# Kernel optimization log

Hardware: AMD Instinct MI355X
Metric: run time of the kernel (lower is better)

The kernel has to match this reference:

```python
import jax, jax.numpy as jnp
import numpy as np

B, T, OMNI_D, STATIC_D = 128, 1024, 32, 16
H = 64            # hidden // 2 (per-direction GRU size)
HID = 128         # hidden
PHYS_LEN, N_PHYS = 432, 5


def _gelu(x):
    return jax.nn.gelu(x, approximate=False)  # torch GELU default = exact erf


def _ln(x, g, b, eps=1e-5):
    m = jnp.mean(x, -1, keepdims=True)
    v = jnp.var(x, -1, keepdims=True)
    return (x - m) / jnp.sqrt(v + eps) * g + b


def _gru_layer(x, Wih, Whh, bih, bhh, reverse):
    # PyTorch GRU cell math; x: [B,T,D] -> (outputs [B,T,H], h_final [B,H])
    Hh = Whh.shape[1]
    gi = jnp.einsum('btd,gd->btg', x, Wih) + bih  # precompute input projections
    if reverse:
        gi = gi[:, ::-1]
    gi = jnp.swapaxes(gi, 0, 1)  # [T,B,3H]
    h0 = jnp.zeros((x.shape[0], Hh), x.dtype)

    def step(h, g):
        gh = h @ Whh.T + bhh
        r = jax.nn.sigmoid(g[:, :Hh] + gh[:, :Hh])
        z = jax.nn.sigmoid(g[:, Hh:2 * Hh] + gh[:, Hh:2 * Hh])
        n = jnp.tanh(g[:, 2 * Hh:] + r * gh[:, 2 * Hh:])
        hn = (1 - z) * n + z * h
        return hn, hn

    hT, ys = jax.lax.scan(step, h0, gi)
    ys = jnp.swapaxes(ys, 0, 1)
    if reverse:
        ys = ys[:, ::-1]
    return ys, hT


def _conv1d(x, W, b, pad, dil):
    y = jax.lax.conv_general_dilated(x, W, (1,), [(pad, pad)], rhs_dilation=(dil,),
                                     dimension_numbers=('NCH', 'OIH', 'NCH'))
    return y + b[None, :, None]


def setup_inputs():
    key = jax.random.key(0)
    ks = iter(jax.random.split(key, 64))

    def rn(shape, s=0.05):
        return jax.random.normal(next(ks), shape, jnp.float32) * s

    inp = {
        'omni_seq': rn((B, T, OMNI_D), 1.0),
        'static_x': rn((B, STATIC_D), 1.0),
        'phys': rn((B, N_PHYS, PHYS_LEN), 1.0),
    }
    for l, d_in in (('l0', OMNI_D), ('l1', 2 * H)):
        for dr in ('f', 'b'):
            inp[f'gru_Wih_{l}{dr}'] = rn((3 * H, d_in))
            inp[f'gru_Whh_{l}{dr}'] = rn((3 * H, H))
            inp[f'gru_bih_{l}{dr}'] = rn((3 * H,))
            inp[f'gru_bhh_{l}{dr}'] = rn((3 * H,))
    inp['sm_W'] = rn((H, STATIC_D)); inp['sm_b'] = rn((H,))
    inp['sm_ln_g'] = jnp.ones((H,), jnp.float32); inp['sm_ln_b'] = jnp.zeros((H,), jnp.float32)
    inp['gate_W'] = rn((N_PHYS, H)); inp['gate_b'] = rn((N_PHYS,))
    inp['attn_in_W'] = rn((3 * N_PHYS, N_PHYS)); inp['attn_in_b'] = rn((3 * N_PHYS,))
    inp['attn_out_W'] = rn((N_PHYS, N_PHYS)); inp['attn_out_b'] = rn((N_PHYS,))
    for i, ksz in ((1, 3), (2, 5), (3, 9)):
        inp[f'conv{i}_W'] = rn((HID // 4, N_PHYS, ksz)); inp[f'conv{i}_b'] = rn((HID // 4,))
    FUSED = HID + H + 3 * (HID // 4)  # 288
    inp['head_ln_g'] = jnp.ones((FUSED,), jnp.float32); inp['head_ln_b'] = jnp.zeros((FUSED,), jnp.float32)
    inp['head_W1'] = rn((HID, FUSED)); inp['head_b1'] = rn((HID,))
    inp['head_W2'] = rn((PHYS_LEN, HID)); inp['head_b2'] = rn((PHYS_LEN,))
    return inp


def reference(omni_seq, static_x, phys,
              gru_Wih_l0f, gru_Whh_l0f, gru_bih_l0f, gru_bhh_l0f,
              gru_Wih_l0b, gru_Whh_l0b, gru_bih_l0b, gru_bhh_l0b,
              gru_Wih_l1f, gru_Whh_l1f, gru_bih_l1f, gru_bhh_l1f,
              gru_Wih_l1b, gru_Whh_l1b, gru_bih_l1b, gru_bhh_l1b,
              sm_W, sm_b, sm_ln_g, sm_ln_b, gate_W, gate_b,
              attn_in_W, attn_in_b, attn_out_W, attn_out_b,
              conv1_W, conv1_b, conv2_W, conv2_b, conv3_W, conv3_b,
              head_ln_g, head_ln_b, head_W1, head_b1, head_W2, head_b2):
    # --- bidirectional 2-layer GRU (eval mode: dropout off) ---
    y0f, _ = _gru_layer(omni_seq, gru_Wih_l0f, gru_Whh_l0f, gru_bih_l0f, gru_bhh_l0f, False)
    y0b, _ = _gru_layer(omni_seq, gru_Wih_l0b, gru_Whh_l0b, gru_bih_l0b, gru_bhh_l0b, True)
    x1 = jnp.concatenate([y0f, y0b], -1)
    _, hf = _gru_layer(x1, gru_Wih_l1f, gru_Whh_l1f, gru_bih_l1f, gru_bhh_l1f, False)
    _, hb = _gru_layer(x1, gru_Wih_l1b, gru_Whh_l1b, gru_bih_l1b, gru_bhh_l1b, True)
    omni_embed = jnp.concatenate([hf, hb], -1)  # h_omni[-2] ++ h_omni[-1], [B,128]
    # --- static MLP ---
    static_embed = _ln(_gelu(static_x @ sm_W.T + sm_b), sm_ln_g, sm_ln_b)  # [B,64]
    # --- gating on phys channels ---
    gates = jax.nn.sigmoid(static_embed @ gate_W.T + gate_b)[..., None]  # [B,5,1]
    p = phys * gates  # [B,5,432]
    # --- tiny MHA: embed_dim=5, 5 heads, head_dim=1 -> scale = 1/sqrt(1) = 1 ---
    pt = jnp.swapaxes(p, 1, 2)  # [B,432,5]
    qkv = pt @ attn_in_W.T + attn_in_b
    E = N_PHYS
    q, k, v = qkv[..., :E], qkv[..., E:2 * E], qkv[..., 2 * E:]
    scores = jnp.einsum('bih,bjh->bhij', q, k)  # [B,5,432,432]
    attn = jax.nn.softmax(scores, -1)
    ao = jnp.einsum('bhij,bjh->bih', attn, v)
    ao = ao @ attn_out_W.T + attn_out_b  # out_proj
    p = jnp.swapaxes(ao, 1, 2)  # [B,5,432]
    # --- dilated conv branches + GELU + adaptive avg pool (= mean over length) ---
    c1 = _gelu(_conv1d(p, conv1_W, conv1_b, 1, 1)).mean(-1)
    c2 = _gelu(_conv1d(p, conv2_W, conv2_b, 2, 2)).mean(-1)
    c3 = _gelu(_conv1d(p, conv3_W, conv3_b, 4, 4)).mean(-1)
    fused = jnp.concatenate([omni_embed, static_embed, c1, c2, c3], 1)  # [B,288]
    h = _ln(fused, head_ln_g, head_ln_b)
    h = _gelu(h @ head_W1.T + head_b1)  # dropout off in eval
    return h @ head_W2.T + head_b2  # [B,432]
```

## Files before the change

### kernel.cpp

```cpp
#include <hip/hip_runtime.h>
#include <stdint.h>

#define B_ 128
#define T_ 1024
#define BT_ (B_*T_)
#define H_ 64
#define G_ 192
#define PL_ 432
#define NP_ 5
#define FUSED_ 288
#define N_IN 41
#define NSTATIC 128
#define NRECUR 256
#define NGEMM 2048

typedef unsigned short u16;
typedef __attribute__((ext_vector_type(8))) short bf16x8;
typedef __attribute__((ext_vector_type(4))) float f32x4;
typedef _Float16 h2 __attribute__((ext_vector_type(2)));
typedef _Float16 h8 __attribute__((ext_vector_type(8)));

__device__ inline float bf2f(u16 u){ union{float f; unsigned int i;} c; c.i = ((unsigned int)u)<<16; return c.f; }
__device__ inline u16 f2bf(float f){ unsigned int u = __float_as_uint(f); unsigned int r = (u + 0x7fffu + ((u>>16)&1u))>>16; return (u16)r; }
__device__ inline _Float16 bf2h(u16 u){ return (_Float16)bf2f(u); }
__device__ inline float sigm(float x){ return 1.f/(1.f+__expf(-x)); }
__device__ inline float tanh_(float x){ float t = __expf(fminf(fmaxf(2.f*x,-30.f),30.f)); return (t-1.f)/(t+1.f); }
__device__ inline float gelu_(float x){ return 0.5f*x*(1.f + erff(x*0.70710678118654752f)); }
__device__ inline float wredsum(float v){
  #pragma unroll
  for(int o=32;o>0;o>>=1) v += __shfl_xor(v,o);
  return v;
}

#if __has_builtin(__builtin_amdgcn_fdot2)
__device__ inline float dot2(h2 a, h2 b, float c){ return __builtin_amdgcn_fdot2(a, b, c, false); }
#else
__device__ inline float dot2(h2 a, h2 b, float c){ return c + (float)a.x*(float)b.x + (float)a.y*(float)b.y; }
#endif

struct CvtArgs {
  const void* src[N_IN];
  unsigned dstOff[N_IN];
  unsigned cnt[N_IN];
  unsigned blkStart[N_IN+1];
};

__global__ __launch_bounds__(256) void convert_k(CvtArgs a, u16* __restrict__ dst,
                                                 unsigned* __restrict__ flags){
  int b = blockIdx.x;
  if ((unsigned)b >= a.blkStart[N_IN]){
    unsigned base = ((unsigned)b - a.blkStart[N_IN])*2048u;
    #pragma unroll
    for(int e=0;e<8;e++){ unsigned idx = base + e*256u + threadIdx.x; if (idx < 4096u) flags[idx] = 0u; }
    return;
  }
  const bool isbf = (((const u16*)a.src[21])[0] == 0x3F80u);
  int lo = 0, hi = N_IN;
  while (hi - lo > 1){ int mid = (lo+hi)>>1; if (a.blkStart[mid] <= (unsigned)b) lo = mid; else hi = mid; }
  const int i = lo;
  const unsigned lb = (unsigned)b - a.blkStart[i];
  const unsigned n = a.cnt[i];
  u16* d = dst + a.dstOff[i];
  if (isbf){
    const u16* s = (const u16*)a.src[i];
    #pragma unroll
    for(int e=0;e<8;e++){ unsigned idx = lb*2048u + e*256u + threadIdx.x; if (idx < n) d[idx] = s[idx]; }
  } else {
    const float* s = (const float*)a.src[i];
    #pragma unroll
    for(int e=0;e<8;e++){ unsigned idx = lb*2048u + e*256u + threadIdx.x; if (idx < n) d[idx] = f2bf(s[idx]); }
  }
}

template<int LAYER>
__device__ void recur_body(int chain, const u16* gi,
    const u16* __restrict__ WhF, const u16* __restrict__ WhB,
    const u16* __restrict__ bhF, const u16* __restrict__ bhB,
    u16* __restrict__ y_x1, float* __restrict__ hfin,
    const unsigned* flags)
{
  const int dir = chain >> 7;
  const int b = chain & 127;
  const int j = threadIdx.x;
  const u16* Wh = dir ? WhB : WhF;
  const u16* bh = dir ? bhB : bhF;

  h2 wr[32], wz[32], wn[32];
  #pragma unroll
  for(int k8=0;k8<8;k8++){
    uint4 q;
    q = *(const uint4*)(Wh + (size_t)j*64 + k8*8);
    wr[4*k8+0] = (h2){bf2h((u16)(q.x&0xffffu)), bf2h((u16)(q.x>>16))};
    wr[4*k8+1] = (h2){bf2h((u16)(q.y&0xffffu)), bf2h((u16)(q.y>>16))};
    wr[4*k8+2] = (h2){bf2h((u16)(q.z&0xffffu)), bf2h((u16)(q.z>>16))};
    wr[4*k8+3] = (h2){bf2h((u16)(q.w&0xffffu)), bf2h((u16)(q.w>>16))};
    q = *(const uint4*)(Wh + (size_t)(64+j)*64 + k8*8);
    wz[4*k8+0] = (h2){bf2h((u16)(q.x&0xffffu)), bf2h((u16)(q.x>>16))};
    wz[4*k8+1] = (h2){bf2h((u16)(q.y&0xffffu)), bf2h((u16)(q.y>>16))};
    wz[4*k8+2] = (h2){bf2h((u16)(q.z&0xffffu)), bf2h((u16)(q.z>>16))};
    wz[4*k8+3] = (h2){bf2h((u16)(q.w&0xffffu)), bf2h((u16)(q.w>>16))};
    q = *(const uint4*)(Wh + (size_t)(128+j)*64 + k8*8);
    wn[4*k8+0] = (h2){bf2h((u16)(q.x&0xffffu)), bf2h((u16)(q.x>>16))};
    wn[4*k8+1] = (h2){bf2h((u16)(q.y&0xffffu)), bf2h((u16)(q.y>>16))};
    wn[4*k8+2] = (h2){bf2h((u16)(q.z&0xffffu)), bf2h((u16)(q.z>>16))};
    wn[4*k8+3] = (h2){bf2h((u16)(q.w&0xffffu)), bf2h((u16)(q.w>>16))};
  }
  const float bhr = bf2f(bh[j]), bhz = bf2f(bh[64+j]), bhn = bf2f(bh[128+j]);

  __shared__ __align__(16) u16 giLds[2][3072];
  __shared__ _Float16 hSf[64];
  h8* hS8 = (h8*)hSf;
  hSf[j] = (_Float16)0.f;

  const u16* giC = gi + (size_t)chain * T_ * G_;

  auto issue_chunk = [&](int c, int buf){
    int tbase = dir ? (1008 - c*16) : (c*16);
    const u16* src = giC + (size_t)tbase*G_ + j*8;
    u16* dst = &giLds[buf][0];
    #pragma unroll
    for(int i=0;i<6;i++){
      __builtin_amdgcn_global_load_lds(
        (const __attribute__((address_space(1))) void*)(src + i*512),
        (__attribute__((address_space(3))) void*)(dst + i*512), 16, 0, 0);
    }
  };

  int readyTile = -1;
  auto wait_tile = [&](int c){
    int tbase = dir ? (1008 - c*16) : (c*16);
    int tile = tbase >> 6;
    if (tile == readyTile) return;
    const unsigned* f = &flags[b*16 + tile];
    while (__hip_atomic_load(f, __ATOMIC_ACQUIRE, __HIP_MEMORY_SCOPE_AGENT) == 0u)
      __builtin_amdgcn_s_sleep(2);
    readyTile = tile;
  };

  wait_tile(0);
  issue_chunk(0, 0);

  float h = 0.f;
  for(int c=0; c<64; ++c){
    if (c < 63) wait_tile(c+1);
    asm volatile("s_waitcnt vmcnt(0)" ::: "memory");
    if (c < 63) issue_chunk(c+1, (c+1)&1);
    const u16* gbuf = &giLds[c&1][0];
    #pragma unroll 2
    for(int ls=0; ls<16; ++ls){
      int row = dir ? (15-ls) : ls;
      const u16* rowp = gbuf + row*G_;
      float r0=bhr, r1=0.f, z0=bhz, z1=0.f, n0=bhn, n1=0.f;
      #pragma unroll
      for(int k=0;k<8;k++){
        h8 hv = hS8[k];
        h2 p0 = __builtin_shufflevector(hv, hv, 0, 1);
        h2 p1 = __builtin_shufflevector(hv, hv, 2, 3);
        h2 p2 = __builtin_shufflevector(hv, hv, 4, 5);
        h2 p3 = __builtin_shufflevector(hv, hv, 6, 7);
        r0 = dot2(wr[4*k+0], p0, r0); r1 = dot2(wr[4*k+1], p1, r1);
        r0 = dot2(wr[4*k+2], p2, r0); r1 = dot2(wr[4*k+3], p3, r1);
        z0 = dot2(wz[4*k+0], p0, z0); z1 = dot2(wz[4*k+1], p1, z1);
        z0 = dot2(wz[4*k+2], p2, z0); z1 = dot2(wz[4*k+3], p3, z1);
        n0 = dot2(wn[4*k+0], p0, n0); n1 = dot2(wn[4*k+1], p1, n1);
        n0 = dot2(wn[4*k+2], p2, n0); n1 = dot2(wn[4*k+3], p3, n1);
      }
      float gr = bf2f(rowp[j]), gz = bf2f(rowp[64+j]), gn = bf2f(rowp[128+j]);

      float r  = sigm(gr + (r0+r1));
      float z  = sigm(gz + (z0+z1));
      float nn = tanh_(gn + r*(n0+n1));
      h = (1.f - z)*nn + z*h;

      hSf[j] = (_Float16)h;

      if (LAYER == 0){
        int s = c*16 + ls;
        int t = dir ? (T_-1-s) : s;
        y_x1[((size_t)b*T_ + t)*128 + dir*64 + j] = f2bf(h);
      }
    }
  }
  if (LAYER == 1) hfin[b*FUSED_ + dir*64 + j] = h;
}

__device__ inline int tile_order(int tslot){ return (tslot & 1) ? (15 - (tslot >> 1)) : (tslot >> 1); }

__device__ inline void publish_flag(unsigned* flags, int idx){
  __syncthreads();
  if (threadIdx.x == 0){
    __threadfence();
    __hip_atomic_store(&flags[idx], 1u, __ATOMIC_RELEASE, __HIP_MEMORY_SCOPE_AGENT);
  }
}

__global__ __launch_bounds__(256,1) void fused0_k(
    const void* __restrict__ Araw,
    const u16* __restrict__ Wf, const u16* __restrict__ Wb,
    const u16* __restrict__ biasF, const u16* __restrict__ biasB,
    u16* gi,
    const u16* __restrict__ WhF, const u16* __restrict__ WhB,
    const u16* __restrict__ bhF, const u16* __restrict__ bhB,
    u16* __restrict__ y_x1, unsigned* flags, const u16* __restrict__ detect)
{
  if (blockIdx.x < NRECUR){
    if (threadIdx.x < 64)
      recur_body<0>(blockIdx.x, gi, WhF, WhB, bhF, bhB, y_x1, nullptr, flags);
    return;
  }
  const bool isbf = (detect[0] == 0x3F80u);
  const int g = blockIdx.x - NRECUR;
  const int bb = g & 127;
  const int ttile = tile_order(g >> 7);
  const int wv = threadIdx.x >> 6, lane = threadIdx.x & 63;
  const int l15 = lane & 15, quad = lane >> 4;
  const size_t mBase = ((size_t)bb*16 + ttile)*64 + wv*16;

  bf16x8 afr;
  if (isbf){
    afr = *(const bf16x8*)((const u16*)Araw + (mBase + l15)*32 + quad*8);
  } else {
    const float* af = (const float*)Araw + (mBase + l15)*32 + quad*8;
    float4 f0 = *(const float4*)af;
    float4 f1 = *(const float4*)(af+4);
    union { bf16x8 v; u16 e[8]; } u_;
    u_.e[0]=f2bf(f0.x); u_.e[1]=f2bf(f0.y); u_.e[2]=f2bf(f0.z); u_.e[3]=f2bf(f0.w);
    u_.e[4]=f2bf(f1.x); u_.e[5]=f2bf(f1.y); u_.e[6]=f2bf(f1.z); u_.e[7]=f2bf(f1.w);
    afr = u_.v;
  }

  #pragma unroll
  for(int half=0; half<2; ++half){
    const u16* W    = half ? Wb : Wf;
    const u16* bias = half ? biasB : biasF;
    u16* o = gi + (size_t)half * BT_ * G_;
    for(int nt=0; nt<12; ++nt){
      int n = nt*16 + l15;
      f32x4 acc = {0.f,0.f,0.f,0.f};
      bf16x8 bfr = *(const bf16x8*)(W + n*32 + quad*8);
      acc = __builtin_amdgcn_mfma_f32_16x16x32_bf16(bfr, afr, acc, 0,0,0);
      ushort4 bb4 = *(const ushort4*)(bias + nt*16 + quad*4);
      ushort4 pk;
      pk.x = f2bf(acc[0] + bf2f(bb4.x));
      pk.y = f2bf(acc[1] + bf2f(bb4.y));
      pk.z = f2bf(acc[2] + bf2f(bb4.z));
      pk.w = f2bf(acc[3] + bf2f(bb4.w));
      *(ushort4*)(o + (mBase + l15)*G_ + nt*16 + quad*4) = pk;
    }
  }
  publish_flag(flags, bb*16 + ttile);
}

template<int KS, int DIL, int PAD>
__device__ inline void do_conv(const float* pS, const u16* Wc, const u16* bc,
                               float* fused, int b, int o, int p, int cslot)
{
  const int Lout = PL_ + 2*PAD - DIL*(KS-1);
  float w[5][KS];
  #pragma unroll
  for(int i=0;i<5;i++)
    #pragma unroll
    for(int t=0;t<KS;t++) w[i][t] = bf2f(Wc[(o*5+i)*KS + t]);
  float bias = bf2f(bc[o]);
  float acc = 0.f;
  for(int l=p; l<Lout; l+=8){
    float s = bias;
    #pragma unroll
    for(int t=0;t<KS;t++){
      int idx = l - PAD + t*DIL;
      if (idx >= 0 && idx < PL_){
        #pragma unroll
        for(int i=0;i<5;i++) s += w[i][t]*pS[i*PL_ + idx];
      }
    }
    acc += gelu_(s);
  }
  #pragma unroll
  for(int off=1;off<8;off<<=1) acc += __shfl_xor(acc,off);
  if (p == 0) fused[b*FUSED_ + 192 + cslot*32 + o] = acc/(float)Lout;
}

__device__ void static_body(int b, int tid,
   const u16* sx, const u16* smW, const u16* smb,
   const u16* lng, const u16* lnb, const u16* gW, const u16* gb,
   const void* physRaw, const u16* aW, const u16* ab,
   const u16* oW, const u16* ob,
   const u16* W1c, const u16* b1c, const u16* W2c, const u16* b2c,
   const u16* W3c, const u16* b3c,
   float* fused, bool isbf)
{
  __shared__ float qS[15*PL_];
  __shared__ float aoS[PL_*5];
  __shared__ float gS[5];
  __shared__ float redS[40];
  __shared__ float kmS[5], knS[5];

  if (tid < 64){
    int j = tid;
    float acc = bf2f(smb[j]);
    #pragma unroll
    for(int k=0;k<16;k++) acc += bf2f(sx[b*16+k])*bf2f(smW[j*16+k]);
    float xg = gelu_(acc);
    float m = wredsum(xg)*(1.f/64.f);
    float d = xg - m;
    float v = wredsum(d*d)*(1.f/64.f);
    float se = d*rsqrtf(v+1e-5f)*bf2f(lng[j]) + bf2f(lnb[j]);
    fused[b*FUSED_ + 128 + j] = se;
    #pragma unroll
    for(int i=0;i<5;i++){
      float p = se*bf2f(gW[i*64+j]);
      float s = wredsum(p);
      if (j == 0) gS[i] = sigm(s + bf2f(gb[i]));
    }
  }
  __syncthreads();

  for(int l=tid; l<PL_; l+=256){
    float pv[5];
    #pragma unroll
    for(int i=0;i<5;i++){
      size_t idx = ((size_t)b*5+i)*PL_ + l;
      float pr = isbf ? bf2f(((const u16*)physRaw)[idx]) : ((const float*)physRaw)[idx];
      pv[i] = pr * gS[i];
    }
    #pragma unroll
    for(int c=0;c<15;c++){
      float a = bf2f(ab[c]);
      #pragma unroll
      for(int i=0;i<5;i++) a += pv[i]*bf2f(aW[c*5+i]);
      qS[c*PL_ + l] = a;
    }
  }
  __syncthreads();

  float mx[5], mn[5];
  #pragma unroll
  for(int h=0;h<5;h++){ mx[h]=-1e30f; mn[h]=1e30f; }
  for(int jj=tid; jj<PL_; jj+=256){
    #pragma unroll
    for(int h=0;h<5;h++){ float kv=qS[(5+h)*PL_+jj]; mx[h]=fmaxf(mx[h],kv); mn[h]=fminf(mn[h],kv); }
  }
  #pragma unroll
  for(int o=32;o>0;o>>=1){
    #pragma unroll
    for(int h=0;h<5;h++){ mx[h]=fmaxf(mx[h],__shfl_xor(mx[h],o)); mn[h]=fminf(mn[h],__shfl_xor(mn[h],o)); }
  }
  int wv = tid>>6;
  if ((tid&63)==0){
    #pragma unroll
    for(int h=0;h<5;h++){ redS[wv*10+h]=mx[h]; redS[wv*10+5+h]=mn[h]; }
  }
  __syncthreads();
  if (tid < 5){
    float a=redS[tid], c=redS[5+tid];
    for(int w2=1;w2<4;w2++){ a=fmaxf(a,redS[w2*10+tid]); c=fminf(c,redS[w2*10+5+tid]); }
    kmS[tid]=a; knS[tid]=c;
  }
  __syncthreads();

  for(int i=tid; i<PL_; i+=256){
    #pragma unroll
    for(int h=0;h<5;h++){
      float s = qS[h*PL_+i];
      float m = fmaxf(s*kmS[h], s*knS[h]);
      const float* kR = &qS[(5+h)*PL_];
      const float* vR = &qS[(10+h)*PL_];
      float den=0.f, num=0.f;
      #pragma unroll 4
      for(int j2=0;j2<PL_;j2++){
        float e = __expf(s*kR[j2]-m);
        den += e; num += e*vR[j2];
      }
      aoS[i*5+h] = num/den;
    }
  }
  __syncthreads();

  float* pS = qS;
  for(int l=tid; l<PL_; l+=256){
    float a[5];
    #pragma unroll
    for(int hh=0;hh<5;hh++) a[hh] = aoS[l*5+hh];
    #pragma unroll
    for(int c=0;c<5;c++){
      float s = bf2f(ob[c]);
      #pragma unroll
      for(int hh=0;hh<5;hh++) s += a[hh]*bf2f(oW[c*5+hh]);
      pS[c*PL_ + l] = s;
    }
  }
  __syncthreads();

  int o = tid >> 3, p = tid & 7;
  do_conv<3,1,1>(pS, W1c, b1c, fused, b, o, p, 0);
  do_conv<5,2,2>(pS, W2c, b2c, fused, b, o, p, 1);
  do_conv<9,4,4>(pS, W3c, b3c, fused, b, o, p, 2);
}

__global__ __launch_bounds__(256,1) void fused1_k(
    const u16* __restrict__ A,
    const u16* __restrict__ Wf, const u16* __restrict__ Wb,
    const u16* __restrict__ biasF, const u16* __restrict__ biasB,
    u16* gi,
    const u16* __restrict__ WhF, const u16* __restrict__ WhB,
    const u16* __restrict__ bhF, const u16* __restrict__ bhB,
    float* __restrict__ fusedOut, unsigned* flags,
    const u16* __restrict__ sx, const u16* __restrict__ smW, const u16* __restrict__ smb,
    const u16* __restrict__ lng, const u16* __restrict__ lnb,
    const u16* __restrict__ gW, const u16* __restrict__ gb,
    const void* __restrict__ physRaw, const u16* __restrict__ aW, const u16* __restrict__ ab,
    const u16* __restrict__ oW, const u16* __restrict__ ob,
    const u16* __restrict__ W1c, const u16* __restrict__ b1c,
    const u16* __restrict__ W2c, const u16* __restrict__ b2c,
    const u16* __restrict__ W3c, const u16* __restrict__ b3c,
    const u16* __restrict__ detect)
{
  const bool isbf = (detect[0] == 0x3F80u);
  if (blockIdx.x < NRECUR){
    if (threadIdx.x < 64)
      recur_body<1>(blockIdx.x, gi, WhF, WhB, bhF, bhB, nullptr, fusedOut, flags);
    return;
  }
  if (blockIdx.x >= NRECUR + NGEMM){
    static_body(blockIdx.x - (NRECUR + NGEMM), threadIdx.x,
                sx, smW, smb, lng, lnb, gW, gb, physRaw, aW, ab,
                oW, ob, W1c, b1c, W2c, b2c, W3c, b3c, fusedOut, isbf);
    return;
  }
  const int g = blockIdx.x - NRECUR;
  const int bb = g & 127;
  const int ttile = tile_order(g >> 7);
  const int wv = threadIdx.x >> 6, lane = threadIdx.x & 63;
  const int l15 = lane & 15, quad = lane >> 4;
  const size_t mBase = ((size_t)bb*16 + ttile)*64 + wv*16;

  bf16x8 afr[4];
  #pragma unroll
  for(int kc=0;kc<4;kc++)
    afr[kc] = *(const bf16x8*)(A + (mBase + l15)*128 + kc*32 + quad*8);

  #pragma unroll
  for(int half=0; half<2; ++half){
    const u16* W    = half ? Wb : Wf;
    const u16* bias = half ? biasB : biasF;
    u16* o = gi + (size_t)half * BT_ * G_;
    for(int nt=0; nt<12; ++nt){
      int n = nt*16 + l15;
      f32x4 acc = {0.f,0.f,0.f,0.f};
      #pragma unroll
      for(int kc=0;kc<4;kc++){
        bf16x8 bfr = *(const bf16x8*)(W + n*128 + kc*32 + quad*8);
        acc = __builtin_amdgcn_mfma_f32_16x16x32_bf16(bfr, afr[kc], acc, 0,0,0);
      }
      ushort4 bb4 = *(const ushort4*)(bias + nt*16 + quad*4);
      ushort4 pk;
      pk.x = f2bf(acc[0] + bf2f(bb4.x));
      pk.y = f2bf(acc[1] + bf2f(bb4.y));
      pk.z = f2bf(acc[2] + bf2f(bb4.z));
      pk.w = f2bf(acc[3] + bf2f(bb4.w));
      *(ushort4*)(o + (mBase + l15)*G_ + nt*16 + quad*4) = pk;
    }
  }
  publish_flag(flags, bb*16 + ttile);
}

__global__ __launch_bounds__(448) void head_k(const float* __restrict__ fused,
   const u16* __restrict__ lng, const u16* __restrict__ lnb,
   const u16* __restrict__ W1, const u16* __restrict__ b1,
   const u16* __restrict__ W2, const u16* __restrict__ b2,
   void* __restrict__ out, const u16* __restrict__ detect)
{
  const bool isbf = (detect[0] == 0x3F80u);
  int b = blockIdx.x, tid = threadIdx.x;
  __shared__ float fS[FUSED_];
  __shared__ float hS[128];
  __shared__ float red[32];
  float v = (tid < FUSED_) ? fused[b*FUSED_ + tid] : 0.f;
  float s1 = wredsum(v);
  float s2 = wredsum(v*v);
  int wv = tid>>6;
  if ((tid&63)==0){ red[wv]=s1; red[8+wv]=s2; }
  __syncthreads();
  if (tid==0){
    float S=0.f, SS=0.f;
    for(int i=0;i<7;i++){ S+=red[i]; SS+=red[8+i]; }
    float m = S/288.f;
    red[16]=m; red[17]=SS/288.f - m*m;
  }
  __syncthreads();
  float m = red[16], var = red[17];
  if (tid < FUSED_) fS[tid] = (v-m)*rsqrtf(var+1e-5f)*bf2f(lng[tid]) + bf2f(lnb[tid]);
  __syncthreads();
  if (tid < 128){
    float a = bf2f(b1[tid]);
    const u16* wr = W1 + (size_t)tid*FUSED_;
    #pragma unroll
    for(int k8=0;k8<36;k8++){
      uint4 q = *(const uint4*)(wr + k8*8);
      a += fS[8*k8+0]*bf2f((u16)(q.x&0xffffu)) + fS[8*k8+1]*bf2f((u16)(q.x>>16))
         + fS[8*k8+2]*bf2f((u16)(q.y&0xffffu)) + fS[8*k8+3]*bf2f((u16)(q.y>>16))
         + fS[8*k8+4]*bf2f((u16)(q.z&0xffffu)) + fS[8*k8+5]*bf2f((u16)(q.z>>16))
         + fS[8*k8+6]*bf2f((u16)(q.w&0xffffu)) + fS[8*k8+7]*bf2f((u16)(q.w>>16));
    }
    hS[tid] = gelu_(a);
  }
  __syncthreads();
  if (tid < PL_){
    float a = bf2f(b2[tid]);
    const u16* wr = W2 + (size_t)tid*128;
    #pragma unroll
    for(int k8=0;k8<16;k8++){
      uint4 q = *(const uint4*)(wr + k8*8);
      a += hS[8*k8+0]*bf2f((u16)(q.x&0xffffu)) + hS[8*k8+1]*bf2f((u16)(q.x>>16))
         + hS[8*k8+2]*bf2f((u16)(q.y&0xffffu)) + hS[8*k8+3]*bf2f((u16)(q.y>>16))
         + hS[8*k8+4]*bf2f((u16)(q.z&0xffffu)) + hS[8*k8+5]*bf2f((u16)(q.z>>16))
         + hS[8*k8+6]*bf2f((u16)(q.w&0xffffu)) + hS[8*k8+7]*bf2f((u16)(q.w>>16));
    }
    size_t oi = (size_t)b*PL_ + tid;
    if (isbf) ((u16*)out)[oi] = f2bf(a);
    else      ((float*)out)[oi] = a;
  }
}

extern "C" void kernel_launch(void* const* d_in, const int* in_sizes, int n_in,
                              void* d_out, int out_size, void* d_ws, size_t ws_size,
                              hipStream_t stream)
{
  static const unsigned cnts[N_IN] = {
    4194304, 2048, 276480,
    6144, 12288, 192, 192,
    6144, 12288, 192, 192,
    24576, 12288, 192, 192,
    24576, 12288, 192, 192,
    1024, 64, 64, 64,
    320, 5,
    75, 15,
    25, 5,
    480, 32, 800, 32, 1440, 32,
    288, 288,
    36864, 128, 55296, 432
  };

  char* ws = (char*)d_ws;
  size_t off = 0;
  auto alloc = [&](size_t bytes){ size_t o = off; off = (off + bytes + 255) & ~(size_t)255; return o; };

  CvtArgs ca;
  const u16* cin[N_IN];
  unsigned totalBlocks = 0;
  for (int i=0;i<N_IN;i++){
    ca.src[i] = d_in[i];
    ca.cnt[i] = cnts[i];
    size_t o = alloc((size_t)cnts[i]*2);
    ca.dstOff[i] = (unsigned)(o/2);
    cin[i] = (const u16*)(ws + o);
    ca.blkStart[i] = totalBlocks;
    if (i != 0 && i != 2) totalBlocks += (cnts[i] + 2047u)/2048u;
  }
  ca.blkStart[N_IN] = totalBlocks;
  u16* canon = (u16*)ws;

  u16*   gi    = (u16*)  (ws + alloc((size_t)2*BT_*G_*2));
  u16*   x1    = (u16*)  (ws + alloc((size_t)BT_*128*2));
  float* fused = (float*)(ws + alloc((size_t)B_*FUSED_*4));
  unsigned* flags = (unsigned*)(ws + alloc((size_t)4096*4));
  (void)ws_size; (void)in_sizes; (void)n_in; (void)out_size;

  convert_k<<<totalBlocks + 2, 256, 0, stream>>>(ca, canon, flags);

  fused0_k<<<NRECUR + NGEMM, 256, 0, stream>>>(d_in[0],
      cin[3], cin[7], cin[5], cin[9], gi,
      cin[4], cin[8], cin[6], cin[10], x1, flags, (const u16*)d_in[21]);

  fused1_k<<<NRECUR + NGEMM + NSTATIC, 256, 0, stream>>>(x1,
      cin[11], cin[15], cin[13], cin[17], gi,
      cin[12], cin[16], cin[14], cin[18], fused, flags + 2048,
      cin[1], cin[19], cin[20], cin[21], cin[22], cin[23], cin[24],
      d_in[2], cin[25], cin[26],
      cin[27], cin[28], cin[29], cin[30], cin[31], cin[32], cin[33], cin[34],
      (const u16*)d_in[21]);

  head_k<<<128, 448, 0, stream>>>(fused, cin[35], cin[36], cin[37], cin[38], cin[39], cin[40],
                                  d_out, (const u16*)d_in[21]);
}
```

Baseline: 1.414 ms.

## Shrink fused GRU/GEMM/static blocks to single-wavefront workgroups

Both fused kernels now launch 64-thread blocks instead of 256. GEMM blocks loop over the four 16-row M sub-tiles inside one wave, and the static branch (attention, out-projection, dilated convs) is rewritten for one wave with fewer LDS buffers and barriers. The aim is to stop recurrence blocks from occupying three idle waves and to let more blocks be resident, which should help the flag-based producer/consumer pipelining. The cost is less parallelism per GEMM and static block, which lengthens the static branch, and the block barrier before the flag publish is removed.

Measured after the change: 1.667 ms. 1.18x slower.

```diff
diff --git a/kernel.cpp b/kernel.cpp
--- a/kernel.cpp
+++ b/kernel.cpp
@@ -187,14 +187,14 @@
 __device__ inline int tile_order(int tslot){ return (tslot & 1) ? (15 - (tslot >> 1)) : (tslot >> 1); }
 
 __device__ inline void publish_flag(unsigned* flags, int idx){
-  __syncthreads();
-  if (threadIdx.x == 0){
-    __threadfence();
+  __threadfence();
+  if (threadIdx.x == 0)
     __hip_atomic_store(&flags[idx], 1u, __ATOMIC_RELEASE, __HIP_MEMORY_SCOPE_AGENT);
-  }
-}
-
-__global__ __launch_bounds__(256,1) void fused0_k(
+}
+
+__global__ __launch_bounds__(64)
+__attribute__((amdgpu_waves_per_eu(1,1)))
+void fused0_k(
     const void* __restrict__ Araw,
     const u16* __restrict__ Wf, const u16* __restrict__ Wb,
     const u16* __restrict__ biasF, const u16* __restrict__ biasB,
@@ -204,56 +204,57 @@
     u16* __restrict__ y_x1, unsigned* flags, const u16* __restrict__ detect)
 {
   if (blockIdx.x < NRECUR){
-    if (threadIdx.x < 64)
-      recur_body<0>(blockIdx.x, gi, WhF, WhB, bhF, bhB, y_x1, nullptr, flags);
+    recur_body<0>(blockIdx.x, gi, WhF, WhB, bhF, bhB, y_x1, nullptr, flags);
     return;
   }
   const bool isbf = (detect[0] == 0x3F80u);
   const int g = blockIdx.x - NRECUR;
   const int bb = g & 127;
   const int ttile = tile_order(g >> 7);
-  const int wv = threadIdx.x >> 6, lane = threadIdx.x & 63;
+  const int lane = threadIdx.x;
   const int l15 = lane & 15, quad = lane >> 4;
-  const size_t mBase = ((size_t)bb*16 + ttile)*64 + wv*16;
-
-  bf16x8 afr;
-  if (isbf){
-    afr = *(const bf16x8*)((const u16*)Araw + (mBase + l15)*32 + quad*8);
-  } else {
-    const float* af = (const float*)Araw + (mBase + l15)*32 + quad*8;
-    float4 f0 = *(const float4*)af;
-    float4 f1 = *(const float4*)(af+4);
-    union { bf16x8 v; u16 e[8]; } u_;
-    u_.e[0]=f2bf(f0.x); u_.e[1]=f2bf(f0.y); u_.e[2]=f2bf(f0.z); u_.e[3]=f2bf(f0.w);
-    u_.e[4]=f2bf(f1.x); u_.e[5]=f2bf(f1.y); u_.e[6]=f2bf(f1.z); u_.e[7]=f2bf(f1.w);
-    afr = u_.v;
-  }
 
   #pragma unroll
-  for(int half=0; half<2; ++half){
-    const u16* W    = half ? Wb : Wf;
-    const u16* bias = half ? biasB : biasF;
-    u16* o = gi + (size_t)half * BT_ * G_;
-    for(int nt=0; nt<12; ++nt){
-      int n = nt*16 + l15;
-      f32x4 acc = {0.f,0.f,0.f,0.f};
-      bf16x8 bfr = *(const bf16x8*)(W + n*32 + quad*8);
-      acc = __builtin_amdgcn_mfma_f32_16x16x32_bf16(bfr, afr, acc, 0,0,0);
-      ushort4 bb4 = *(const ushort4*)(bias + nt*16 + quad*4);
-      ushort4 pk;
-      pk.x = f2bf(acc[0] + bf2f(bb4.x));
-      pk.y = f2bf(acc[1] + bf2f(bb4.y));
-      pk.z = f2bf(acc[2] + bf2f(bb4.z));
-      pk.w = f2bf(acc[3] + bf2f(bb4.w));
-      *(ushort4*)(o + (mBase + l15)*G_ + nt*16 + quad*4) = pk;
+  for(int m0=0;m0<4;m0++){
+    const size_t mBase = ((size_t)bb*16 + ttile)*64 + m0*16;
+    bf16x8 afr;
+    if (isbf){
+      afr = *(const bf16x8*)((const u16*)Araw + (mBase + l15)*32 + quad*8);
+    } else {
+      const float* af = (const float*)Araw + (mBase + l15)*32 + quad*8;
+      float4 f0 = *(const float4*)af;
+      float4 f1 = *(const float4*)(af+4);
+      union { bf16x8 v; u16 e[8]; } u_;
+      u_.e[0]=f2bf(f0.x); u_.e[1]=f2bf(f0.y); u_.e[2]=f2bf(f0.z); u_.e[3]=f2bf(f0.w);
+      u_.e[4]=f2bf(f1.x); u_.e[5]=f2bf(f1.y); u_.e[6]=f2bf(f1.z); u_.e[7]=f2bf(f1.w);
+      afr = u_.v;
+    }
+    #pragma unroll
+    for(int half=0; half<2; ++half){
+      const u16* W    = half ? Wb : Wf;
+      const u16* bias = half ? biasB : biasF;
+      u16* o = gi + (size_t)half * BT_ * G_;
+      for(int nt=0; nt<12; ++nt){
+        int n = nt*16 + l15;
+        f32x4 acc = {0.f,0.f,0.f,0.f};
+        bf16x8 bfr = *(const bf16x8*)(W + n*32 + quad*8);
+        acc = __builtin_amdgcn_mfma_f32_16x16x32_bf16(bfr, afr, acc, 0,0,0);
+        ushort4 bb4 = *(const ushort4*)(bias + nt*16 + quad*4);
+        ushort4 pk;
+        pk.x = f2bf(acc[0] + bf2f(bb4.x));
+        pk.y = f2bf(acc[1] + bf2f(bb4.y));
+        pk.z = f2bf(acc[2] + bf2f(bb4.z));
+        pk.w = f2bf(acc[3] + bf2f(bb4.w));
+        *(ushort4*)(o + (mBase + l15)*G_ + nt*16 + quad*4) = pk;
+      }
     }
   }
   publish_flag(flags, bb*16 + ttile);
 }
 
 template<int KS, int DIL, int PAD>
-__device__ inline void do_conv(const float* pS, const u16* Wc, const u16* bc,
-                               float* fused, int b, int o, int p, int cslot)
+__device__ inline void do_conv64(const float* pS, const u16* Wc, const u16* bc,
+                                 float* fused, int b, int o, int p, int cslot)
 {
   const int Lout = PL_ + 2*PAD - DIL*(KS-1);
   float w[5][KS];
@@ -263,7 +264,7 @@
     for(int t=0;t<KS;t++) w[i][t] = bf2f(Wc[(o*5+i)*KS + t]);
   float bias = bf2f(bc[o]);
   float acc = 0.f;
-  for(int l=p; l<Lout; l+=8){
+  for(int l=p; l<Lout; l+=2){
     float s = bias;
     #pragma unroll
     for(int t=0;t<KS;t++){
@@ -275,8 +276,7 @@
     }
     acc += gelu_(s);
   }
-  #pragma unroll
-  for(int off=1;off<8;off<<=1) acc += __shfl_xor(acc,off);
+  acc += __shfl_xor(acc, 32);
   if (p == 0) fused[b*FUSED_ + 192 + cslot*32 + o] = acc/(float)Lout;
 }
 
@@ -290,12 +290,10 @@
    float* fused, bool isbf)
 {
   __shared__ float qS[15*PL_];
-  __shared__ float aoS[PL_*5];
   __shared__ float gS[5];
-  __shared__ float redS[40];
   __shared__ float kmS[5], knS[5];
 
-  if (tid < 64){
+  {
     int j = tid;
     float acc = bf2f(smb[j]);
     #pragma unroll
@@ -315,7 +313,7 @@
   }
   __syncthreads();
 
-  for(int l=tid; l<PL_; l+=256){
+  for(int l=tid; l<PL_; l+=64){
     float pv[5];
     #pragma unroll
     for(int i=0;i<5;i++){
@@ -333,35 +331,30 @@
   }
   __syncthreads();
 
-  float mx[5], mn[5];
-  #pragma unroll
-  for(int h=0;h<5;h++){ mx[h]=-1e30f; mn[h]=1e30f; }
-  for(int jj=tid; jj<PL_; jj+=256){
-    #pragma unroll
-    for(int h=0;h<5;h++){ float kv=qS[(5+h)*PL_+jj]; mx[h]=fmaxf(mx[h],kv); mn[h]=fminf(mn[h],kv); }
-  }
-  #pragma unroll
-  for(int o=32;o>0;o>>=1){
-    #pragma unroll
-    for(int h=0;h<5;h++){ mx[h]=fmaxf(mx[h],__shfl_xor(mx[h],o)); mn[h]=fminf(mn[h],__shfl_xor(mn[h],o)); }
-  }
-  int wv = tid>>6;
-  if ((tid&63)==0){
-    #pragma unroll
-    for(int h=0;h<5;h++){ redS[wv*10+h]=mx[h]; redS[wv*10+5+h]=mn[h]; }
-  }
-  __syncthreads();
-  if (tid < 5){
-    float a=redS[tid], c=redS[5+tid];
-    for(int w2=1;w2<4;w2++){ a=fmaxf(a,redS[w2*10+tid]); c=fminf(c,redS[w2*10+5+tid]); }
-    kmS[tid]=a; knS[tid]=c;
-  }
-  __syncthreads();
-
-  for(int i=tid; i<PL_; i+=256){
+  {
+    float mx[5], mn[5];
+    #pragma unroll
+    for(int h=0;h<5;h++){ mx[h]=-1e30f; mn[h]=1e30f; }
+    for(int jj=tid; jj<PL_; jj+=64){
+      #pragma unroll
+      for(int h=0;h<5;h++){ float kv=qS[(5+h)*PL_+jj]; mx[h]=fmaxf(mx[h],kv); mn[h]=fminf(mn[h],kv); }
+    }
+    #pragma unroll
+    for(int o=32;o>0;o>>=1){
+      #pragma unroll
+      for(int h=0;h<5;h++){ mx[h]=fmaxf(mx[h],__shfl_xor(mx[h],o)); mn[h]=fminf(mn[h],__shfl_xor(mn[h],o)); }
+    }
+    if (tid < 5){ kmS[tid]=mx[tid]; knS[tid]=mn[tid]; }
+  }
+  __syncthreads();
+
+  for(int l=tid; l<PL_; l+=64){
+    float qv[5], aov[5];
+    #pragma unroll
+    for(int h=0;h<5;h++) qv[h] = qS[h*PL_+l];
     #pragma unroll
     for(int h=0;h<5;h++){
-      float s = qS[h*PL_+i];
+      float s = qv[h];
       float m = fmaxf(s*kmS[h], s*knS[h]);
       const float* kR = &qS[(5+h)*PL_];
       const float* vR = &qS[(10+h)*PL_];
@@ -371,33 +364,27 @@
         float e = __expf(s*kR[j2]-m);
         den += e; num += e*vR[j2];
       }
-      aoS[i*5+h] = num/den;
-    }
-  }
-  __syncthreads();
-
-  float* pS = qS;
-  for(int l=tid; l<PL_; l+=256){
-    float a[5];
-    #pragma unroll
-    for(int hh=0;hh<5;hh++) a[hh] = aoS[l*5+hh];
+      aov[h] = num/den;
+    }
     #pragma unroll
     for(int c=0;c<5;c++){
       float s = bf2f(ob[c]);
       #pragma unroll
-      for(int hh=0;hh<5;hh++) s += a[hh]*bf2f(oW[c*5+hh]);
-      pS[c*PL_ + l] = s;
-    }
-  }
-  __syncthreads();
-
-  int o = tid >> 3, p = tid & 7;
-  do_conv<3,1,1>(pS, W1c, b1c, fused, b, o, p, 0);
-  do_conv<5,2,2>(pS, W2c, b2c, fused, b, o, p, 1);
-  do_conv<9,4,4>(pS, W3c, b3c, fused, b, o, p, 2);
-}
-
-__global__ __launch_bounds__(256,1) void fused1_k(
+      for(int hh=0;hh<5;hh++) s += aov[hh]*bf2f(oW[c*5+hh]);
+      qS[c*PL_ + l] = s;
+    }
+  }
+  __syncthreads();
+
+  int o = tid & 31, p = tid >> 5;
+  do_conv64<3,1,1>(qS, W1c, b1c, fused, b, o, p, 0);
+  do_conv64<5,2,2>(qS, W2c, b2c, fused, b, o, p, 1);
+  do_conv64<9,4,4>(qS, W3c, b3c, fused, b, o, p, 2);
+}
+
+__global__ __launch_bounds__(64)
+__attribute__((amdgpu_waves_per_eu(1,1)))
+void fused1_k(
     const u16* __restrict__ A,
     const u16* __restrict__ Wf, const u16* __restrict__ Wb,
     const u16* __restrict__ biasF, const u16* __restrict__ biasB,
@@ -417,8 +404,7 @@
 {
   const bool isbf = (detect[0] == 0x3F80u);
   if (blockIdx.x < NRECUR){
-    if (threadIdx.x < 64)
-      recur_body<1>(blockIdx.x, gi, WhF, WhB, bhF, bhB, nullptr, fusedOut, flags);
+    recur_body<1>(blockIdx.x, gi, WhF, WhB, bhF, bhB, nullptr, fusedOut, flags);
     return;
   }
   if (blockIdx.x >= NRECUR + NGEMM){
@@ -430,35 +416,37 @@
   const int g = blockIdx.x - NRECUR;
   const int bb = g & 127;
   const int ttile = tile_order(g >> 7);
-  const int wv = threadIdx.x >> 6, lane = threadIdx.x & 63;
+  const int lane = threadIdx.x;
   const int l15 = lane & 15, quad = lane >> 4;
-  const size_t mBase = ((size_t)bb*16 + ttile)*64 + wv*16;
-
-  bf16x8 afr[4];
+
   #pragma unroll
-  for(int kc=0;kc<4;kc++)
-    afr[kc] = *(const bf16x8*)(A + (mBase + l15)*128 + kc*32 + quad*8);
-
-  #pragma unroll
-  for(int half=0; half<2; ++half){
-    const u16* W    = half ? Wb : Wf;
-    const u16* bias = half ? biasB : biasF;
-    u16* o = gi + (size_t)half * BT_ * G_;
-    for(int nt=0; nt<12; ++nt){
-      int n = nt*16 + l15;
-      f32x4 acc = {0.f,0.f,0.f,0.f};
-      #pragma unroll
-      for(int kc=0;kc<4;kc++){
-        bf16x8 bfr = *(const bf16x8*)(W + n*128 + kc*32 + quad*8);
-        acc = __builtin_amdgcn_mfma_f32_16x16x32_bf16(bfr, afr[kc], acc, 0,0,0);
+  for(int m0=0;m0<4;m0++){
+    const size_t mBase = ((size_t)bb*16 + ttile)*64 + m0*16;
+    bf16x8 afr[4];
+    #pragma unroll
+    for(int kc=0;kc<4;kc++)
+      afr[kc] = *(const bf16x8*)(A + (mBase + l15)*128 + kc*32 + quad*8);
+    #pragma unroll
+    for(int half=0; half<2; ++half){
+      const u16* W    = half ? Wb : Wf;
+      const u16* bias = half ? biasB : biasF;
+      u16* o = gi + (size_t)half * BT_ * G_;
+      for(int nt=0; nt<12; ++nt){
+        int n = nt*16 + l15;
+        f32x4 acc = {0.f,0.f,0.f,0.f};
+        #pragma unroll
+        for(int kc=0;kc<4;kc++){
+          bf16x8 bfr = *(const bf16x8*)(W + n*128 + kc*32 + quad*8);
+          acc = __builtin_amdgcn_mfma_f32_16x16x32_bf16(bfr, afr[kc], acc, 0,0,0);
+        }
+        ushort4 bb4 = *(const ushort4*)(bias + nt*16 + quad*4);
+        ushort4 pk;
+        pk.x = f2bf(acc[0] + bf2f(bb4.x));
+        pk.y = f2bf(acc[1] + bf2f(bb4.y));
+        pk.z = f2bf(acc[2] + bf2f(bb4.z));
+        pk.w = f2bf(acc[3] + bf2f(bb4.w));
+        *(ushort4*)(o + (mBase + l15)*G_ + nt*16 + quad*4) = pk;
       }
-      ushort4 bb4 = *(const ushort4*)(bias + nt*16 + quad*4);
-      ushort4 pk;
-      pk.x = f2bf(acc[0] + bf2f(bb4.x));
-      pk.y = f2bf(acc[1] + bf2f(bb4.y));
-      pk.z = f2bf(acc[2] + bf2f(bb4.z));
-      pk.w = f2bf(acc[3] + bf2f(bb4.w));
-      *(ushort4*)(o + (mBase + l15)*G_ + nt*16 + quad*4) = pk;
     }
   }
   publish_flag(flags, bb*16 + ttile);
@@ -568,11 +556,11 @@
 
   convert_k<<<totalBlocks + 2, 256, 0, stream>>>(ca, canon, flags);
 
-  fused0_k<<<NRECUR + NGEMM, 256, 0, stream>>>(d_in[0],
+  fused0_k<<<NRECUR + NGEMM, 64, 0, stream>>>(d_in[0],
       cin[3], cin[7], cin[5], cin[9], gi,
       cin[4], cin[8], cin[6], cin[10], x1, flags, (const u16*)d_in[21]);
 
-  fused1_k<<<NRECUR + NGEMM + NSTATIC, 256, 0, stream>>>(x1,
+  fused1_k<<<NRECUR + NGEMM + NSTATIC, 64, 0, stream>>>(x1,
       cin[11], cin[15], cin[13], cin[17], gi,
       cin[12], cin[16], cin[14], cin[18], fused, flags + 2048,
       cin[1], cin[19], cin[20], cin[21], cin[22], cin[23], cin[24],
```
